# Kernel tuning notes

Hardware: AMD Instinct MI355X
Metric: run time of the kernel (lower is better)

The kernel has to match this reference:

```python
import jax, jax.numpy as jnp
import numpy as np

L, D, I, H, B, T, NBLK = 2, 2048, 5632, 16, 2, 1024, 4
EPS, TEMP, THETA = 1e-6, 1.0, 10000.0


def _rms_base(x):
    # RMSNorm without affine weight, computed in fp32 (matches _rms_norm_base)
    x = x.astype(jnp.float32)
    return x * jax.lax.rsqrt(jnp.mean(x * x, axis=-1, keepdims=True) + EPS)


def _rope(x):
    # x: [B,T,H,dh], rotate-half RoPE
    dh = x.shape[-1]
    inv = 1.0 / (THETA ** (jnp.arange(0, dh, 2, dtype=jnp.float32) / dh))
    t = jnp.arange(x.shape[1], dtype=jnp.float32)
    fr = jnp.outer(t, inv)  # [T, dh/2]
    cos = jnp.tile(jnp.cos(fr), (1, 2))[None, :, None, :]
    sin = jnp.tile(jnp.sin(fr), (1, 2))[None, :, None, :]
    x1, x2 = jnp.split(x, 2, axis=-1)
    return x * cos + jnp.concatenate([-x2, x1], axis=-1) * sin


def _attention(x, Wq, Wk, Wv, Wo):
    Bb, Tt, Dd = x.shape
    dh = Dd // H
    q = _rope((x @ Wq).reshape(Bb, Tt, H, dh))
    k = _rope((x @ Wk).reshape(Bb, Tt, H, dh))
    v = (x @ Wv).reshape(Bb, Tt, H, dh)
    s = jnp.einsum('bqhd,bkhd->bhqk', q, k) / jnp.sqrt(jnp.float32(dh))
    causal = jnp.tril(jnp.ones((Tt, Tt), bool))
    s = jnp.where(causal, s, jnp.float32(-1e30))
    a = jax.nn.softmax(s, axis=-1)
    return jnp.einsum('bhqk,bkhd->bqhd', a, v).reshape(Bb, Tt, Dd) @ Wo


def _forward(block_states, w_query_attn, key_norm_w_attn, w_query_mlp, key_norm_w_mlp,
             attn_norm_w, Wq, Wk, Wv, Wo, mlp_norm_w, Wgate, Wup, Wdown,
             active_mask, current_block_idx):
    n, Bb, Tt, Dd = block_states.shape
    scale = jnp.sqrt(jnp.float32(Dd)) * TEMP
    block_input = block_states[current_block_idx]
    mask = active_mask.astype(jnp.float32)[:, None, None]  # [B,1,1]

    # ---- phase 1: batch_attend_completed_blocks over all 2L routers ----
    # effective query = w_query * key_norm.weight (norm weight folded into query)
    q_eff = jnp.stack([w_query_attn * key_norm_w_attn,
                       w_query_mlp * key_norm_w_mlp], axis=1).reshape(2 * L, Dd)
    base_keys = _rms_base(block_states)                      # [n,B,T,D] fp32
    scores = jnp.einsum('qd,nbtd->qnbt', q_eff, base_keys) / scale
    mx = scores.max(axis=1)                                  # [q,B,T]
    ex = jnp.exp(scores - mx[:, None])                       # [q,n,B,T]
    lse = ex.sum(axis=1)                                     # [q,B,T]
    outs = jnp.einsum('qnbt,nbtd->qbtd', ex, block_states)   # unnormalized

    def merge(qi, partial):
        # merge_with_partial_block: online-softmax merge of phase1 stats with
        # the score of the current partial block
        if partial is None:
            return outs[qi] / lse[qi][..., None]
        ps = jnp.einsum('d,btd->bt', q_eff[qi], _rms_base(partial)) / scale
        m = jnp.maximum(mx[qi], ps)
        c1 = jnp.exp(mx[qi] - m)
        c2 = jnp.exp(ps - m)
        denom = c1 * lse[qi] + c2
        return (outs[qi] * (c1 * lse[qi] / denom)[..., None]
                + partial * (c2 / denom)[..., None])

    def blend(old, new):
        return new * mask + old * (1.0 - mask)

    def rmsn(x, w):
        return _rms_base(x) * w

    partial = None
    for i in range(L):
        attn_in = merge(2 * i, partial)
        attn_out = _attention(rmsn(attn_in, attn_norm_w[i]), Wq[i], Wk[i], Wv[i], Wo[i])
        old = block_input if partial is None else partial
        partial = blend(old, attn_out if partial is None else partial + attn_out)
        mlp_in = merge(2 * i + 1, partial)
        h = rmsn(mlp_in, mlp_norm_w[i])
        mlp_out = (jax.nn.silu(h @ Wgate[i]) * (h @ Wup[i])) @ Wdown[i]
        partial = blend(partial, partial + mlp_out)
    return partial


def setup_inputs() -> dict:
    key = jax.random.key(0)
    ks = jax.random.split(key, 12)
    p = lambda k, shape: jax.random.normal(k, shape, jnp.float32) * 0.02
    return {
        'block_states': jax.random.normal(ks[0], (NBLK, B, T, D), jnp.float32),
        'active_mask': jnp.ones((B,), bool),
        'w_query_attn': jax.random.normal(ks[1], (L, D), jnp.float32) * 0.02,
        'key_norm_w_attn': jnp.ones((L, D), jnp.float32),
        'w_query_mlp': jax.random.normal(ks[2], (L, D), jnp.float32) * 0.02,
        'key_norm_w_mlp': jnp.ones((L, D), jnp.float32),
        'attn_norm_w': jnp.ones((L, D), jnp.float32),
        'Wq': p(ks[3], (L, D, D)), 'Wk': p(ks[4], (L, D, D)),
        'Wv': p(ks[5], (L, D, D)), 'Wo': p(ks[6], (L, D, D)),
        'mlp_norm_w': jnp.ones((L, D), jnp.float32),
        'Wgate': p(ks[7], (L, D, I)), 'Wup': p(ks[8], (L, D, I)),
        'Wdown': p(ks[9], (L, I, D)),
        'current_block_idx': 3,
    }


def reference(block_states, active_mask, w_query_attn, key_norm_w_attn, w_query_mlp,
              key_norm_w_mlp, attn_norm_w, Wq, Wk, Wv, Wo, mlp_norm_w,
              Wgate, Wup, Wdown, current_block_idx):
    return _forward(block_states, w_query_attn, key_norm_w_attn, w_query_mlp,
                    key_norm_w_mlp, attn_norm_w, Wq, Wk, Wv, Wo, mlp_norm_w,
                    Wgate, Wup, Wdown, active_mask, current_block_idx)
```

## Files before the change

kernel.cpp:

```cpp
#include <hip/hip_runtime.h>

typedef unsigned short u16;
typedef __bf16 bf16x8 __attribute__((ext_vector_type(8)));
typedef float f32x4 __attribute__((ext_vector_type(4)));

__device__ __forceinline__ float u2f(unsigned int b){ union{unsigned int u; float f;} x; x.u=b; return x.f; }
__device__ __forceinline__ u16 f2b(float f){
  union{float fv; unsigned int u;} x; x.fv=f;
  unsigned int r = x.u + 0x7fffu + ((x.u>>16)&1u);
  return (u16)(r>>16);
}
__device__ __forceinline__ float b2f(u16 v){ return u2f(((unsigned int)v)<<16); }
__device__ __forceinline__ void load8(const float* p, float* o){
  float4 a = ((const float4*)p)[0], b = ((const float4*)p)[1];
  o[0]=a.x;o[1]=a.y;o[2]=a.z;o[3]=a.w;o[4]=b.x;o[5]=b.y;o[6]=b.z;o[7]=b.w;
}

#define INV_SCALE 0.022097086912079608f
#define ATT_SCALE 0.08838834764831845f

__global__ __launch_bounds__(256) void transpose_cast(const float* __restrict__ src, u16* __restrict__ dst, int K, int N)
{
  __shared__ u16 tile[64][68];
  size_t plane = (size_t)K * N * blockIdx.z;
  src += plane; dst += plane;
  int kb = blockIdx.y*64, nb = blockIdx.x*64;
  int t = threadIdx.x;
  int c4 = (t&15)*4, r0 = t>>4;
  #pragma unroll
  for (int p=0;p<4;p++){
    int kk = r0 + p*16;
    float4 v = *(const float4*)(src + (size_t)(kb+kk)*N + nb + c4);
    tile[kk][c4]=f2b(v.x); tile[kk][c4+1]=f2b(v.y); tile[kk][c4+2]=f2b(v.z); tile[kk][c4+3]=f2b(v.w);
  }
  __syncthreads();
  #pragma unroll
  for (int p=0;p<4;p++){
    int nn = r0 + p*16;
    ushort4 v;
    v.x=tile[c4][nn]; v.y=tile[c4+1][nn]; v.z=tile[c4+2][nn]; v.w=tile[c4+3][nn];
    *(ushort4*)(dst + (size_t)(nb+nn)*K + kb + c4) = v;
  }
}

__global__ __launch_bounds__(256) void phase1_kernel(
    const float* __restrict__ bs, const float* __restrict__ wqa, const float* __restrict__ kna,
    const float* __restrict__ wqm, const float* __restrict__ knm,
    float* __restrict__ outs, float* __restrict__ mxb, float* __restrict__ lseb)
{
  const int D=2048, M=2048;
  int m = blockIdx.x, t = threadIdx.x;
  int col = t*8;
  float x[4][8];
  #pragma unroll
  for (int n=0;n<4;n++) load8(bs + ((size_t)n*M + m)*D + col, x[n]);
  float qe[4][8];
  {
    float a[8], b[8];
    load8(wqa+col,a);   load8(kna+col,b);
    #pragma unroll
    for (int j=0;j<8;j++) qe[0][j]=a[j]*b[j];
    load8(wqm+col,a);   load8(knm+col,b);
    #pragma unroll
    for (int j=0;j<8;j++) qe[1][j]=a[j]*b[j];
    load8(wqa+D+col,a); load8(kna+D+col,b);
    #pragma unroll
    for (int j=0;j<8;j++) qe[2][j]=a[j]*b[j];
    load8(wqm+D+col,a); load8(knm+D+col,b);
    #pragma unroll
    for (int j=0;j<8;j++) qe[3][j]=a[j]*b[j];
  }
  float vals[20];
  #pragma unroll
  for (int n=0;n<4;n++){
    float s=0.f;
    #pragma unroll
    for (int j=0;j<8;j++) s += x[n][j]*x[n][j];
    vals[n]=s;
  }
  #pragma unroll
  for (int q=0;q<4;q++)
    #pragma unroll
    for (int n=0;n<4;n++){
      float s=0.f;
      #pragma unroll
      for (int j=0;j<8;j++) s += qe[q][j]*x[n][j];
      vals[4+q*4+n]=s;
    }
  #pragma unroll
  for (int s=0;s<20;s++){
    float v=vals[s];
    v+=__shfl_xor(v,1,64); v+=__shfl_xor(v,2,64); v+=__shfl_xor(v,4,64);
    v+=__shfl_xor(v,8,64); v+=__shfl_xor(v,16,64); v+=__shfl_xor(v,32,64);
    vals[s]=v;
  }
  __shared__ float red[20][4];
  int w=t>>6, lane=t&63;
  if (lane==0){
    #pragma unroll
    for (int s=0;s<20;s++) red[s][w]=vals[s];
  }
  __syncthreads();
  float tot[20];
  #pragma unroll
  for (int s=0;s<20;s++) tot[s]=red[s][0]+red[s][1]+red[s][2]+red[s][3];
  float rn[4];
  #pragma unroll
  for (int n=0;n<4;n++) rn[n]=rsqrtf(tot[n]*(1.0f/2048.0f)+1e-6f);
  #pragma unroll
  for (int q=0;q<4;q++){
    float s0=tot[4+q*4+0]*rn[0]*INV_SCALE;
    float s1=tot[4+q*4+1]*rn[1]*INV_SCALE;
    float s2=tot[4+q*4+2]*rn[2]*INV_SCALE;
    float s3=tot[4+q*4+3]*rn[3]*INV_SCALE;
    float mx=fmaxf(fmaxf(s0,s1),fmaxf(s2,s3));
    float e0=__expf(s0-mx), e1=__expf(s1-mx), e2=__expf(s2-mx), e3=__expf(s3-mx);
    float lse=e0+e1+e2+e3;
    if (t==0){ mxb[(size_t)q*M+m]=mx; lseb[(size_t)q*M+m]=lse; }
    float* op = outs + ((size_t)q*M+m)*(size_t)D + col;
    float4 v0, v1;
    v0.x=e0*x[0][0]+e1*x[1][0]+e2*x[2][0]+e3*x[3][0];
    v0.y=e0*x[0][1]+e1*x[1][1]+e2*x[2][1]+e3*x[3][1];
    v0.z=e0*x[0][2]+e1*x[1][2]+e2*x[2][2]+e3*x[3][2];
    v0.w=e0*x[0][3]+e1*x[1][3]+e2*x[2][3]+e3*x[3][3];
    v1.x=e0*x[0][4]+e1*x[1][4]+e2*x[2][4]+e3*x[3][4];
    v1.y=e0*x[0][5]+e1*x[1][5]+e2*x[2][5]+e3*x[3][5];
    v1.z=e0*x[0][6]+e1*x[1][6]+e2*x[2][6]+e3*x[3][6];
    v1.w=e0*x[0][7]+e1*x[1][7]+e2*x[2][7]+e3*x[3][7];
    ((float4*)op)[0]=v0; ((float4*)op)[1]=v1;
  }
}

__global__ __launch_bounds__(256) void merge_norm_kernel(
    const float* __restrict__ outs_q, const float* __restrict__ mx_q, const float* __restrict__ lse_q,
    const float* __restrict__ partial, const float* __restrict__ wq, const float* __restrict__ kn,
    const float* __restrict__ nw, int has_partial, u16* __restrict__ xnorm)
{
  const int D=2048;
  int m = blockIdx.x, t = threadIdx.x, col = t*8;
  size_t row = (size_t)m*D + col;
  float o[8];
  load8(outs_q+row, o);
  float mx = mx_q[m], lse = lse_q[m];
  float mg[8];
  __shared__ float red[3][4];
  int w=t>>6, lane=t&63;
  if (has_partial){
    float p[8];
    load8(partial+row, p);
    float qv[8], kv[8];
    load8(wq+col,qv); load8(kn+col,kv);
    float ss=0.f, dp=0.f;
    #pragma unroll
    for (int j=0;j<8;j++){ ss += p[j]*p[j]; dp += qv[j]*kv[j]*p[j]; }
    #pragma unroll
    for (int msk=1; msk<64; msk<<=1){ ss += __shfl_xor(ss,msk,64); dp += __shfl_xor(dp,msk,64); }
    if (lane==0){ red[0][w]=ss; red[1][w]=dp; }
    __syncthreads();
    ss = red[0][0]+red[0][1]+red[0][2]+red[0][3];
    dp = red[1][0]+red[1][1]+red[1][2]+red[1][3];
    float ps = dp * rsqrtf(ss*(1.0f/2048.0f)+1e-6f) * INV_SCALE;
    float mm = fmaxf(mx, ps);
    float c1 = __expf(mx-mm), c2 = __expf(ps-mm);
    float denom = c1*lse + c2;
    float fo = c1*lse/denom, fp = c2/denom;
    #pragma unroll
    for (int j=0;j<8;j++) mg[j] = o[j]*fo + p[j]*fp;
  } else {
    float inv = 1.0f/lse;
    #pragma unroll
    for (int j=0;j<8;j++) mg[j] = o[j]*inv;
  }
  float ssm=0.f;
  #pragma unroll
  for (int j=0;j<8;j++) ssm += mg[j]*mg[j];
  #pragma unroll
  for (int msk=1; msk<64; msk<<=1) ssm += __shfl_xor(ssm,msk,64);
  if (lane==0) red[2][w]=ssm;
  __syncthreads();
  ssm = red[2][0]+red[2][1]+red[2][2]+red[2][3];
  float r = rsqrtf(ssm*(1.0f/2048.0f)+1e-6f);
  float wv[8]; load8(nw+col, wv);
  ushort4 o0, o1;
  o0.x=f2b(mg[0]*r*wv[0]); o0.y=f2b(mg[1]*r*wv[1]); o0.z=f2b(mg[2]*r*wv[2]); o0.w=f2b(mg[3]*r*wv[3]);
  o1.x=f2b(mg[4]*r*wv[4]); o1.y=f2b(mg[5]*r*wv[5]); o1.z=f2b(mg[6]*r*wv[6]); o1.w=f2b(mg[7]*r*wv[7]);
  ((ushort4*)(xnorm+row))[0]=o0; ((ushort4*)(xnorm+row))[1]=o1;
}

template<int BN, bool F32OUT>
__global__ __launch_bounds__(256) void gemm_tn(
    const u16* __restrict__ Abase, const u16* __restrict__ BTbase, size_t btz,
    u16* __restrict__ Cbb, size_t cbz, float* __restrict__ Cf, int beta, int N, int K)
{
  constexpr int WNT = BN/32;
  constexpr int BCH = BN/32;
  __shared__ bf16x8 As[8][130];
  __shared__ bf16x8 Bs[8][BN+2];
  const u16* A  = Abase  + (size_t)blockIdx.y*128*K;
  const u16* BT = BTbase + btz*blockIdx.z + (size_t)blockIdx.x*BN*K;
  int tid = threadIdx.x;
  int wv = tid>>6, lane = tid&63, quad = lane>>4, l16 = lane&15;
  int wm = (wv&1)*64, wn = (wv>>1)*(BN/2);
  f32x4 acc[4][WNT];
  #pragma unroll
  for (int i=0;i<4;i++)
    #pragma unroll
    for (int j=0;j<WNT;j++){ f32x4 z={0.f,0.f,0.f,0.f}; acc[i][j]=z; }
  for (int kt=0; kt<K; kt+=64){
    #pragma unroll
    for (int p=0;p<4;p++){
      int lin = p*256+tid; int kq = lin&7, mm = lin>>3;
      As[kq][mm] = *(const bf16x8*)(A + (size_t)mm*K + kt + kq*8);
    }
    #pragma unroll
    for (int p=0;p<BCH;p++){
      int lin = p*256+tid; int kq = lin&7, nn = lin>>3;
      Bs[kq][nn] = *(const bf16x8*)(BT + (size_t)nn*K + kt + kq*8);
    }
    __syncthreads();
    #pragma unroll
    for (int kk=0;kk<2;kk++){
      bf16x8 af[4], bfr[WNT];
      #pragma unroll
      for (int mi=0;mi<4;mi++) af[mi] = As[kk*4+quad][wm+mi*16+l16];
      #pragma unroll
      for (int ni=0;ni<WNT;ni++) bfr[ni] = Bs[kk*4+quad][wn+ni*16+l16];
      #pragma unroll
      for (int mi=0;mi<4;mi++)
        #pragma unroll
        for (int ni=0;ni<WNT;ni++)
          acc[mi][ni] = __builtin_amdgcn_mfma_f32_16x16x32_bf16(af[mi], bfr[ni], acc[mi][ni], 0,0,0);
    }
    __syncthreads();
  }
  int row0 = blockIdx.y*128 + wm + quad*4;
  int col0 = blockIdx.x*BN + wn + l16;
  if (F32OUT){
    #pragma unroll
    for (int mi=0;mi<4;mi++)
      #pragma unroll
      for (int ni=0;ni<WNT;ni++)
        #pragma unroll
        for (int r=0;r<4;r++){
          size_t idx = (size_t)(row0+mi*16+r)*N + (col0+ni*16);
          float pv = beta ? Cf[idx] : 0.0f;
          Cf[idx] = pv + acc[mi][ni][r];
        }
  } else {
    u16* Cb = Cbb + cbz*blockIdx.z;
    #pragma unroll
    for (int mi=0;mi<4;mi++)
      #pragma unroll
      for (int ni=0;ni<WNT;ni++)
        #pragma unroll
        for (int r=0;r<4;r++){
          size_t idx = (size_t)(row0+mi*16+r)*N + (col0+ni*16);
          Cb[idx] = f2b(acc[mi][ni][r]);
        }
  }
}

__global__ __launch_bounds__(256,2) void gemm_gateup(
    const u16* __restrict__ Abase, const u16* __restrict__ Gb, const u16* __restrict__ Ub,
    u16* __restrict__ HG, int N, int K)
{
  __shared__ bf16x8 As[8][130];
  __shared__ bf16x8 Gs[8][130];
  __shared__ bf16x8 Us[8][130];
  const u16* A = Abase + (size_t)blockIdx.y*128*K;
  const u16* G = Gb + (size_t)blockIdx.x*128*K;
  const u16* U = Ub + (size_t)blockIdx.x*128*K;
  int tid = threadIdx.x;
  int wv = tid>>6, lane = tid&63, quad = lane>>4, l16 = lane&15;
  int wm = (wv&1)*64, wn = (wv>>1)*64;
  f32x4 ag[4][4], au[4][4];
  #pragma unroll
  for (int i=0;i<4;i++)
    #pragma unroll
    for (int j=0;j<4;j++){ f32x4 z={0.f,0.f,0.f,0.f}; ag[i][j]=z; au[i][j]=z; }
  for (int kt=0; kt<K; kt+=64){
    #pragma unroll
    for (int p=0;p<4;p++){
      int lin = p*256+tid; int kq = lin&7, mm = lin>>3;
      As[kq][mm] = *(const bf16x8*)(A + (size_t)mm*K + kt + kq*8);
      Gs[kq][mm] = *(const bf16x8*)(G + (size_t)mm*K + kt + kq*8);
      Us[kq][mm] = *(const bf16x8*)(U + (size_t)mm*K + kt + kq*8);
    }
    __syncthreads();
    #pragma unroll
    for (int kk=0;kk<2;kk++){
      bf16x8 af[4], gf[4], uf[4];
      #pragma unroll
      for (int mi=0;mi<4;mi++) af[mi] = As[kk*4+quad][wm+mi*16+l16];
      #pragma unroll
      for (int ni=0;ni<4;ni++){ gf[ni] = Gs[kk*4+quad][wn+ni*16+l16]; uf[ni] = Us[kk*4+quad][wn+ni*16+l16]; }
      #pragma unroll
      for (int mi=0;mi<4;mi++)
        #pragma unroll
        for (int ni=0;ni<4;ni++){
          ag[mi][ni] = __builtin_amdgcn_mfma_f32_16x16x32_bf16(af[mi], gf[ni], ag[mi][ni], 0,0,0);
          au[mi][ni] = __builtin_amdgcn_mfma_f32_16x16x32_bf16(af[mi], uf[ni], au[mi][ni], 0,0,0);
        }
    }
    __syncthreads();
  }
  int row0 = blockIdx.y*128 + wm + quad*4;
  int col0 = blockIdx.x*128 + wn + l16;
  #pragma unroll
  for (int mi=0;mi<4;mi++)
    #pragma unroll
    for (int ni=0;ni<4;ni++)
      #pragma unroll
      for (int r=0;r<4;r++){
        float g = ag[mi][ni][r], u = au[mi][ni][r];
        float h = g/(1.0f+__expf(-g))*u;
        HG[(size_t)(row0+mi*16+r)*N + (col0+ni*16)] = f2b(h);
      }
}

__global__ __launch_bounds__(256) void rope_kernel(u16* __restrict__ qb, u16* __restrict__ kb)
{
  int idx = blockIdx.x*256 + threadIdx.x;
  int j  = idx & 63;
  int h  = (idx>>6) & 15;
  int bt = idx >> 10;
  int t  = bt & 1023;
  float inv = __expf(-(float)j * (9.210340371976184f/64.0f));
  float fr = (float)t * inv;
  float cs = cosf(fr), sn = sinf(fr);
  size_t base = (size_t)bt*2048 + h*128 + j;
  float x1 = b2f(qb[base]), x2 = b2f(qb[base+64]);
  qb[base]    = f2b(x1*cs - x2*sn);
  qb[base+64] = f2b(x2*cs + x1*sn);
  x1 = b2f(kb[base]); x2 = b2f(kb[base+64]);
  kb[base]    = f2b(x1*cs - x2*sn);
  kb[base+64] = f2b(x2*cs + x1*sn);
}

__global__ __launch_bounds__(256) void attn_kernel(
    const u16* __restrict__ q, const u16* __restrict__ k, const u16* __restrict__ v,
    u16* __restrict__ o)
{
  const int T=1024, D=2048;
  int qt = blockIdx.x;
  int b = blockIdx.y>>4, h = blockIdx.y&15;
  __shared__ bf16x8 Qs[16][67];
  __shared__ bf16x8 Ks[16][67];
  __shared__ bf16x8 Vs[8][130];
  __shared__ bf16x8 Ps[4][8][16];
  int tid=threadIdx.x, w=tid>>6, lane=tid&63, quad=lane>>4, l16=lane&15;
  size_t qbase = ((size_t)(b*T + qt*64))*D + h*128;
  #pragma unroll
  for (int p=0;p<4;p++){
    int lin=p*256+tid; int kq=lin&15, qr=lin>>4;
    Qs[kq][qr] = *(const bf16x8*)(q + qbase + (size_t)qr*D + kq*8);
  }
  f32x4 oacc[8];
  #pragma unroll
  for (int i=0;i<8;i++){ f32x4 z={0.f,0.f,0.f,0.f}; oacc[i]=z; }
  float mi[4], li[4];
  #pragma unroll
  for (int r=0;r<4;r++){ mi[r]=-INFINITY; li[r]=0.f; }
  for (int kt=0; kt<=qt; kt++){
    __syncthreads();
    size_t kbase = ((size_t)(b*T + kt*64))*D + h*128;
    #pragma unroll
    for (int p=0;p<4;p++){
      int lin=p*256+tid; int kq=lin&15, kr=lin>>4;
      Ks[kq][kr] = *(const bf16x8*)(k + kbase + (size_t)kr*D + kq*8);
    }
    #pragma unroll
    for (int p=0;p<4;p++){
      int lin=p*256+tid; int d=lin&127, kq=lin>>7;
      union{ bf16x8 v8; u16 u[8]; } tmp;
      #pragma unroll
      for (int j=0;j<8;j++) tmp.u[j] = v[kbase + (size_t)(kq*8+j)*D + d];
      Vs[kq][d] = tmp.v8;
    }
    __syncthreads();
    f32x4 s[4];
    #pragma unroll
    for (int ni=0;ni<4;ni++){ f32x4 z={0.f,0.f,0.f,0.f}; s[ni]=z; }
    #pragma unroll
    for (int kk=0;kk<4;kk++){
      bf16x8 a = Qs[kk*4+quad][w*16+l16];
      #pragma unroll
      for (int ni=0;ni<4;ni++)
        s[ni] = __builtin_amdgcn_mfma_f32_16x16x32_bf16(a, Ks[kk*4+quad][ni*16+l16], s[ni], 0,0,0);
    }
    int qrow = qt*64 + w*16 + quad*4;
    #pragma unroll
    for (int ni=0;ni<4;ni++)
      #pragma unroll
      for (int r=0;r<4;r++){
        float val = s[ni][r]*ATT_SCALE;
        int kc = kt*64 + ni*16 + l16;
        if (kc > qrow + r) val = -1e30f;
        s[ni][r] = val;
      }
    float rmax[4];
    #pragma unroll
    for (int r=0;r<4;r++) rmax[r] = fmaxf(fmaxf(s[0][r],s[1][r]), fmaxf(s[2][r],s[3][r]));
    #pragma unroll
    for (int r=0;r<4;r++){
      rmax[r]=fmaxf(rmax[r],__shfl_xor(rmax[r],1,64));
      rmax[r]=fmaxf(rmax[r],__shfl_xor(rmax[r],2,64));
      rmax[r]=fmaxf(rmax[r],__shfl_xor(rmax[r],4,64));
      rmax[r]=fmaxf(rmax[r],__shfl_xor(rmax[r],8,64));
    }
    float mnew[4], alpha[4], rsum[4];
    #pragma unroll
    for (int r=0;r<4;r++) mnew[r]=fmaxf(mi[r],rmax[r]);
    #pragma unroll
    for (int ni=0;ni<4;ni++)
      #pragma unroll
      for (int r=0;r<4;r++) s[ni][r]=__expf(s[ni][r]-mnew[r]);
    #pragma unroll
    for (int r=0;r<4;r++){
      rsum[r]=s[0][r]+s[1][r]+s[2][r]+s[3][r];
      rsum[r]+=__shfl_xor(rsum[r],1,64);
      rsum[r]+=__shfl_xor(rsum[r],2,64);
      rsum[r]+=__shfl_xor(rsum[r],4,64);
      rsum[r]+=__shfl_xor(rsum[r],8,64);
      alpha[r]=__expf(mi[r]-mnew[r]);
      li[r]=li[r]*alpha[r]+rsum[r];
      mi[r]=mnew[r];
    }
    u16* Pp = (u16*)&Ps[w][0][0];
    #pragma unroll
    for (int ni=0;ni<4;ni++)
      #pragma unroll
      for (int r=0;r<4;r++){
        int kc = ni*16+l16;
        Pp[(((kc>>3)*16) + quad*4 + r)*8 + (kc&7)] = f2b(s[ni][r]);
      }
    __syncthreads();
    #pragma unroll
    for (int dn=0;dn<8;dn++){
      oacc[dn][0]*=alpha[0]; oacc[dn][1]*=alpha[1];
      oacc[dn][2]*=alpha[2]; oacc[dn][3]*=alpha[3];
    }
    #pragma unroll
    for (int kk2=0;kk2<2;kk2++){
      bf16x8 pa = Ps[w][kk2*4+quad][l16];
      #pragma unroll
      for (int dn=0;dn<8;dn++)
        oacc[dn] = __builtin_amdgcn_mfma_f32_16x16x32_bf16(pa, Vs[kk2*4+quad][dn*16+l16], oacc[dn], 0,0,0);
    }
  }
  size_t obase = ((size_t)(b*T + qt*64 + w*16 + quad*4))*D + h*128 + l16;
  #pragma unroll
  for (int dn=0;dn<8;dn++)
    #pragma unroll
    for (int r=0;r<4;r++)
      o[obase + (size_t)r*D + dn*16] = f2b(oacc[dn][r]/li[r]);
}

__global__ __launch_bounds__(256) void copy_kernel(const float* __restrict__ p, float* __restrict__ o)
{
  int idx = blockIdx.x*256 + threadIdx.x;
  ((float4*)o)[idx] = ((const float4*)p)[idx];
}

extern "C" void kernel_launch(void* const* d_in, const int* in_sizes, int n_in,
                              void* d_out, int out_size, void* d_ws, size_t ws_size,
                              hipStream_t stream) {
  (void)in_sizes; (void)n_in; (void)out_size; (void)ws_size;
  const size_t D=2048, I=5632, M=2048;
  const size_t MD=M*D, MI=M*I, LDD=2*D*D, LDI=2*D*I;

  const float* bs  = (const float*)d_in[0];
  const float* wqa = (const float*)d_in[2];
  const float* kna = (const float*)d_in[3];
  const float* wqm = (const float*)d_in[4];
  const float* knm = (const float*)d_in[5];
  const float* anw = (const float*)d_in[6];
  const float* Wq  = (const float*)d_in[7];
  const float* Wk  = (const float*)d_in[8];
  const float* Wv  = (const float*)d_in[9];
  const float* Wo  = (const float*)d_in[10];
  const float* mnw = (const float*)d_in[11];
  const float* Wg  = (const float*)d_in[12];
  const float* Wu  = (const float*)d_in[13];
  const float* Wd  = (const float*)d_in[14];

  char* wsp = (char*)d_ws;
  auto alloc = [&](size_t bytes){ char* p = wsp; wsp += (bytes + 255) & ~(size_t)255; return p; };
  u16*   WTqkv  = (u16*)  alloc(3*LDD*2);
  u16*   WTo    = (u16*)  alloc(LDD*2);
  u16*   WTg    = (u16*)  alloc(LDI*2);
  u16*   WTu    = (u16*)  alloc(LDI*2);
  u16*   WTd    = (u16*)  alloc(LDI*2);
  float* outs   = (float*)alloc(4*MD*4);
  float* mxb    = (float*)alloc(4*M*4);
  float* lseb   = (float*)alloc(4*M*4);
  float* partial= (float*)alloc(MD*4);
  u16*   xnorm  = (u16*)  alloc(MD*2);
  u16*   qkv    = (u16*)  alloc(3*MD*2);
  u16*   attno  = (u16*)  alloc(MD*2);
  u16*   hg     = (u16*)  alloc(MI*2);

  transpose_cast<<<dim3(32,32,2),256,0,stream>>>(Wq, WTqkv,        2048, 2048);
  transpose_cast<<<dim3(32,32,2),256,0,stream>>>(Wk, WTqkv+LDD,    2048, 2048);
  transpose_cast<<<dim3(32,32,2),256,0,stream>>>(Wv, WTqkv+2*LDD,  2048, 2048);
  transpose_cast<<<dim3(32,32,2),256,0,stream>>>(Wo, WTo,          2048, 2048);
  transpose_cast<<<dim3(88,32,2),256,0,stream>>>(Wg, WTg,          2048, 5632);
  transpose_cast<<<dim3(88,32,2),256,0,stream>>>(Wu, WTu,          2048, 5632);
  transpose_cast<<<dim3(32,88,2),256,0,stream>>>(Wd, WTd,          5632, 2048);

  phase1_kernel<<<2048,256,0,stream>>>(bs, wqa, kna, wqm, knm, outs, mxb, lseb);

  for (int i=0;i<2;i++){
    merge_norm_kernel<<<2048,256,0,stream>>>(outs + (size_t)(2*i)*MD, mxb + (size_t)(2*i)*M,
        lseb + (size_t)(2*i)*M, partial, wqa + i*D, kna + i*D, anw + i*D, i>0?1:0, xnorm);
    gemm_tn<128,false><<<dim3(16,16,3),256,0,stream>>>(xnorm, WTqkv + (size_t)i*D*D, LDD,
        qkv, MD, nullptr, 0, 2048, 2048);
    rope_kernel<<<8192,256,0,stream>>>(qkv, qkv+MD);
    attn_kernel<<<dim3(16,32),256,0,stream>>>(qkv, qkv+MD, qkv+2*MD, attno);
    gemm_tn<64,true><<<dim3(32,16,1),256,0,stream>>>(attno, WTo + (size_t)i*D*D, 0,
        nullptr, 0, partial, i>0?1:0, 2048, 2048);
    merge_norm_kernel<<<2048,256,0,stream>>>(outs + (size_t)(2*i+1)*MD, mxb + (size_t)(2*i+1)*M,
        lseb + (size_t)(2*i+1)*M, partial, wqm + i*D, knm + i*D, mnw + i*D, 1, xnorm);
    gemm_gateup<<<dim3(44,16),256,0,stream>>>(xnorm, WTg + (size_t)i*I*D, WTu + (size_t)i*I*D,
        hg, 5632, 2048);
    gemm_tn<64,true><<<dim3(32,16,1),256,0,stream>>>(hg, WTd + (size_t)i*D*I, 0,
        nullptr, 0, partial, 1, 2048, 5632);
  }
  copy_kernel<<<4096,256,0,stream>>>(partial, (float*)d_out);
}
```

Baseline: 1.349 ms.

## Use direct global-to-LDS loads with XOR swizzle and pre-transposed V

Replaces register-staged global→LDS copies in the GEMM and attention kernels with global_load_lds direct transfers, using an XOR-swizzled row-major LDS layout to avoid bank conflicts on the MFMA fragment reads. Adds a V transpose kernel so attention loads V in 16-byte contiguous chunks instead of gathering 8 scalar strided loads per element. This cuts VGPR traffic and uncoalesced reads, at the cost of an extra transpose pass and reliance on correct swizzle indexing.

```diff
diff --git a/kernel.cpp b/kernel.cpp
--- a/kernel.cpp
+++ b/kernel.cpp
@@ -14,6 +14,10 @@
 __device__ __forceinline__ void load8(const float* p, float* o){
   float4 a = ((const float4*)p)[0], b = ((const float4*)p)[1];
   o[0]=a.x;o[1]=a.y;o[2]=a.z;o[3]=a.w;o[4]=b.x;o[5]=b.y;o[6]=b.z;o[7]=b.w;
+}
+__device__ __forceinline__ void gl_lds16(const u16* g, bf16x8* l){
+  __builtin_amdgcn_global_load_lds((const __attribute__((address_space(1))) void*)g,
+                                   (__attribute__((address_space(3))) void*)l, 16, 0, 0);
 }
 
 #define INV_SCALE 0.022097086912079608f
@@ -40,6 +44,31 @@
     ushort4 v;
     v.x=tile[c4][nn]; v.y=tile[c4+1][nn]; v.z=tile[c4+2][nn]; v.w=tile[c4+3][nn];
     *(ushort4*)(dst + (size_t)(nb+nn)*K + kb + c4) = v;
+  }
+}
+
+__global__ __launch_bounds__(256) void vtrans_kernel(const u16* __restrict__ v, u16* __restrict__ vT)
+{
+  __shared__ u16 tile[64][68];
+  int b = blockIdx.z>>4, h = blockIdx.z&15;
+  int t0 = blockIdx.x*64, d0 = blockIdx.y*64;
+  int t = threadIdx.x;
+  int c4 = (t&15)*4, r0 = t>>4;
+  const u16* src = v + ((size_t)(b*1024) + t0)*2048 + h*128 + d0;
+  #pragma unroll
+  for (int p=0;p<4;p++){
+    int tt = r0 + p*16;
+    ushort4 val = *(const ushort4*)(src + (size_t)tt*2048 + c4);
+    tile[tt][c4]=val.x; tile[tt][c4+1]=val.y; tile[tt][c4+2]=val.z; tile[tt][c4+3]=val.w;
+  }
+  __syncthreads();
+  u16* dst = vT + ((size_t)blockIdx.z*128 + d0)*1024 + t0;
+  #pragma unroll
+  for (int p=0;p<4;p++){
+    int dd = r0 + p*16;
+    ushort4 o;
+    o.x=tile[c4][dd]; o.y=tile[c4+1][dd]; o.z=tile[c4+2][dd]; o.w=tile[c4+3][dd];
+    *(ushort4*)(dst + (size_t)dd*1024 + c4) = o;
   }
 }
 
@@ -193,14 +222,14 @@
     u16* __restrict__ Cbb, size_t cbz, float* __restrict__ Cf, int beta, int N, int K)
 {
   constexpr int WNT = BN/32;
-  constexpr int BCH = BN/32;
-  __shared__ bf16x8 As[8][130];
-  __shared__ bf16x8 Bs[8][BN+2];
+  __shared__ bf16x8 As[1024];
+  __shared__ bf16x8 Bs[BN*8];
   const u16* A  = Abase  + (size_t)blockIdx.y*128*K;
   const u16* BT = BTbase + btz*blockIdx.z + (size_t)blockIdx.x*BN*K;
   int tid = threadIdx.x;
   int wv = tid>>6, lane = tid&63, quad = lane>>4, l16 = lane&15;
   int wm = (wv&1)*64, wn = (wv>>1)*(BN/2);
+  int wbase = tid & ~63;
   f32x4 acc[4][WNT];
   #pragma unroll
   for (int i=0;i<4;i++)
@@ -209,22 +238,23 @@
   for (int kt=0; kt<K; kt+=64){
     #pragma unroll
     for (int p=0;p<4;p++){
-      int lin = p*256+tid; int kq = lin&7, mm = lin>>3;
-      As[kq][mm] = *(const bf16x8*)(A + (size_t)mm*K + kt + kq*8);
-    }
-    #pragma unroll
-    for (int p=0;p<BCH;p++){
-      int lin = p*256+tid; int kq = lin&7, nn = lin>>3;
-      Bs[kq][nn] = *(const bf16x8*)(BT + (size_t)nn*K + kt + kq*8);
+      int s = p*256+tid; int mm = s>>3; int kq = (s&7) ^ (mm&7);
+      gl_lds16(A + (size_t)mm*K + kt + kq*8, &As[p*256 + wbase]);
+    }
+    #pragma unroll
+    for (int p=0;p<BN/32;p++){
+      int s = p*256+tid; int nn = s>>3; int kq = (s&7) ^ (nn&7);
+      gl_lds16(BT + (size_t)nn*K + kt + kq*8, &Bs[p*256 + wbase]);
     }
     __syncthreads();
     #pragma unroll
     for (int kk=0;kk<2;kk++){
+      int xq = (kk*4+quad) ^ (l16&7);
       bf16x8 af[4], bfr[WNT];
       #pragma unroll
-      for (int mi=0;mi<4;mi++) af[mi] = As[kk*4+quad][wm+mi*16+l16];
-      #pragma unroll
-      for (int ni=0;ni<WNT;ni++) bfr[ni] = Bs[kk*4+quad][wn+ni*16+l16];
+      for (int mi=0;mi<4;mi++) af[mi] = As[(wm+mi*16+l16)*8 + xq];
+      #pragma unroll
+      for (int ni=0;ni<WNT;ni++) bfr[ni] = Bs[(wn+ni*16+l16)*8 + xq];
       #pragma unroll
       for (int mi=0;mi<4;mi++)
         #pragma unroll
@@ -264,15 +294,16 @@
     const u16* __restrict__ Abase, const u16* __restrict__ Gb, const u16* __restrict__ Ub,
     u16* __restrict__ HG, int N, int K)
 {
-  __shared__ bf16x8 As[8][130];
-  __shared__ bf16x8 Gs[8][130];
-  __shared__ bf16x8 Us[8][130];
+  __shared__ bf16x8 As[1024];
+  __shared__ bf16x8 Gs[1024];
+  __shared__ bf16x8 Us[1024];
   const u16* A = Abase + (size_t)blockIdx.y*128*K;
   const u16* G = Gb + (size_t)blockIdx.x*128*K;
   const u16* U = Ub + (size_t)blockIdx.x*128*K;
   int tid = threadIdx.x;
   int wv = tid>>6, lane = tid&63, quad = lane>>4, l16 = lane&15;
   int wm = (wv&1)*64, wn = (wv>>1)*64;
+  int wbase = tid & ~63;
   f32x4 ag[4][4], au[4][4];
   #pragma unroll
   for (int i=0;i<4;i++)
@@ -281,19 +312,21 @@
   for (int kt=0; kt<K; kt+=64){
     #pragma unroll
     for (int p=0;p<4;p++){
-      int lin = p*256+tid; int kq = lin&7, mm = lin>>3;
-      As[kq][mm] = *(const bf16x8*)(A + (size_t)mm*K + kt + kq*8);
-      Gs[kq][mm] = *(const bf16x8*)(G + (size_t)mm*K + kt + kq*8);
-      Us[kq][mm] = *(const bf16x8*)(U + (size_t)mm*K + kt + kq*8);
+      int s = p*256+tid; int mm = s>>3; int kq = (s&7) ^ (mm&7);
+      size_t off = (size_t)mm*K + kt + kq*8;
+      gl_lds16(A + off, &As[p*256 + wbase]);
+      gl_lds16(G + off, &Gs[p*256 + wbase]);
+      gl_lds16(U + off, &Us[p*256 + wbase]);
     }
     __syncthreads();
     #pragma unroll
     for (int kk=0;kk<2;kk++){
+      int xq = (kk*4+quad) ^ (l16&7);
       bf16x8 af[4], gf[4], uf[4];
       #pragma unroll
-      for (int mi=0;mi<4;mi++) af[mi] = As[kk*4+quad][wm+mi*16+l16];
-      #pragma unroll
-      for (int ni=0;ni<4;ni++){ gf[ni] = Gs[kk*4+quad][wn+ni*16+l16]; uf[ni] = Us[kk*4+quad][wn+ni*16+l16]; }
+      for (int mi=0;mi<4;mi++) af[mi] = As[(wm+mi*16+l16)*8 + xq];
+      #pragma unroll
+      for (int ni=0;ni<4;ni++){ gf[ni] = Gs[(wn+ni*16+l16)*8 + xq]; uf[ni] = Us[(wn+ni*16+l16)*8 + xq]; }
       #pragma unroll
       for (int mi=0;mi<4;mi++)
         #pragma unroll
@@ -338,22 +371,25 @@
 }
 
 __global__ __launch_bounds__(256) void attn_kernel(
-    const u16* __restrict__ q, const u16* __restrict__ k, const u16* __restrict__ v,
+    const u16* __restrict__ q, const u16* __restrict__ k, const u16* __restrict__ vT,
     u16* __restrict__ o)
 {
   const int T=1024, D=2048;
   int qt = blockIdx.x;
-  int b = blockIdx.y>>4, h = blockIdx.y&15;
-  __shared__ bf16x8 Qs[16][67];
-  __shared__ bf16x8 Ks[16][67];
-  __shared__ bf16x8 Vs[8][130];
+  int b = blockIdx.y>>4;
+  __shared__ bf16x8 Qs[1024];
+  __shared__ bf16x8 Ks[1024];
+  __shared__ bf16x8 Vs[1024];
   __shared__ bf16x8 Ps[4][8][16];
   int tid=threadIdx.x, w=tid>>6, lane=tid&63, quad=lane>>4, l16=lane&15;
+  int wbase = tid & ~63;
+  int h = blockIdx.y & 15;
   size_t qbase = ((size_t)(b*T + qt*64))*D + h*128;
+  const u16* vtp = vT + (size_t)blockIdx.y*128*1024;
   #pragma unroll
   for (int p=0;p<4;p++){
-    int lin=p*256+tid; int kq=lin&15, qr=lin>>4;
-    Qs[kq][qr] = *(const bf16x8*)(q + qbase + (size_t)qr*D + kq*8);
+    int s=p*256+tid; int qr=s>>4; int kq=(s&15) ^ (qr&15);
+    gl_lds16(q + qbase + (size_t)qr*D + kq*8, &Qs[p*256 + wbase]);
   }
   f32x4 oacc[8];
   #pragma unroll
@@ -366,16 +402,13 @@
     size_t kbase = ((size_t)(b*T + kt*64))*D + h*128;
     #pragma unroll
     for (int p=0;p<4;p++){
-      int lin=p*256+tid; int kq=lin&15, kr=lin>>4;
-      Ks[kq][kr] = *(const bf16x8*)(k + kbase + (size_t)kr*D + kq*8);
+      int s=p*256+tid; int kr=s>>4; int kq=(s&15) ^ (kr&15);
+      gl_lds16(k + kbase + (size_t)kr*D + kq*8, &Ks[p*256 + wbase]);
     }
     #pragma unroll
     for (int p=0;p<4;p++){
-      int lin=p*256+tid; int d=lin&127, kq=lin>>7;
-      union{ bf16x8 v8; u16 u[8]; } tmp;
-      #pragma unroll
-      for (int j=0;j<8;j++) tmp.u[j] = v[kbase + (size_t)(kq*8+j)*D + d];
-      Vs[kq][d] = tmp.v8;
+      int s=p*256+tid; int d=s>>3; int kq=(s&7) ^ (d&7);
+      gl_lds16(vtp + (size_t)d*1024 + kt*64 + kq*8, &Vs[p*256 + wbase]);
     }
     __syncthreads();
     f32x4 s[4];
@@ -383,10 +416,11 @@
     for (int ni=0;ni<4;ni++){ f32x4 z={0.f,0.f,0.f,0.f}; s[ni]=z; }
     #pragma unroll
     for (int kk=0;kk<4;kk++){
-      bf16x8 a = Qs[kk*4+quad][w*16+l16];
+      int xq = (kk*4+quad) ^ l16;
+      bf16x8 a = Qs[(w*16+l16)*16 + xq];
       #pragma unroll
       for (int ni=0;ni<4;ni++)
-        s[ni] = __builtin_amdgcn_mfma_f32_16x16x32_bf16(a, Ks[kk*4+quad][ni*16+l16], s[ni], 0,0,0);
+        s[ni] = __builtin_amdgcn_mfma_f32_16x16x32_bf16(a, Ks[(ni*16+l16)*16 + xq], s[ni], 0,0,0);
     }
     int qrow = qt*64 + w*16 + quad*4;
     #pragma unroll
@@ -442,10 +476,11 @@
     }
     #pragma unroll
     for (int kk2=0;kk2<2;kk2++){
+      int xv = (kk2*4+quad) ^ (l16&7);
       bf16x8 pa = Ps[w][kk2*4+quad][l16];
       #pragma unroll
       for (int dn=0;dn<8;dn++)
-        oacc[dn] = __builtin_amdgcn_mfma_f32_16x16x32_bf16(pa, Vs[kk2*4+quad][dn*16+l16], oacc[dn], 0,0,0);
+        oacc[dn] = __builtin_amdgcn_mfma_f32_16x16x32_bf16(pa, Vs[(dn*16+l16)*8 + xv], oacc[dn], 0,0,0);
     }
   }
   size_t obase = ((size_t)(b*T + qt*64 + w*16 + quad*4))*D + h*128 + l16;
@@ -497,6 +532,7 @@
   float* partial= (float*)alloc(MD*4);
   u16*   xnorm  = (u16*)  alloc(MD*2);
   u16*   qkv    = (u16*)  alloc(3*MD*2);
+  u16*   vt     = (u16*)  alloc(MD*2);
   u16*   attno  = (u16*)  alloc(MD*2);
   u16*   hg     = (u16*)  alloc(MI*2);
 
@@ -516,7 +552,8 @@
     gemm_tn<128,false><<<dim3(16,16,3),256,0,stream>>>(xnorm, WTqkv + (size_t)i*D*D, LDD,
         qkv, MD, nullptr, 0, 2048, 2048);
     rope_kernel<<<8192,256,0,stream>>>(qkv, qkv+MD);
-    attn_kernel<<<dim3(16,32),256,0,stream>>>(qkv, qkv+MD, qkv+2*MD, attno);
+    vtrans_kernel<<<dim3(16,2,32),256,0,stream>>>(qkv+2*MD, vt);
+    attn_kernel<<<dim3(16,32),256,0,stream>>>(qkv, qkv+MD, vt, attno);
     gemm_tn<64,true><<<dim3(32,16,1),256,0,stream>>>(attno, WTo + (size_t)i*D*D, 0,
         nullptr, 0, partial, i>0?1:0, 2048, 2048);
     merge_norm_kernel<<<2048,256,0,stream>>>(outs + (size_t)(2*i+1)*MD, mxb + (size_t)(2*i+1)*M,
```

After: 1.259 ms. -6.6%, faster.
